# Optimization experiments

Hardware: AMD Instinct MI355X
Metric: run time of the kernel (lower is better)

The kernel has to match this reference:

```python
import jax, jax.numpy as jnp
import numpy as np

B, N_SNPS, N_GENES = 16, 500000, 20000
N_NODES, N_EDGES = 600000, 320000
NF, L = 8, 2
BN_EPS = 1e-5

def bn(x, g, b):
    # eval-mode BatchNorm1d with freshly-initialized running stats (mean=0, var=1)
    return x * jax.lax.rsqrt(jnp.float32(1.0) + BN_EPS) * g + b

def gelu(x):
    return jax.nn.gelu(x, approximate=False)  # torch F.gelu default (erf)

def setup_inputs():
    key = jax.random.key(0)
    ks = iter(jax.random.split(key, 40))
    nk = lambda: next(ks)
    lin = lambda kk, i, o: jax.random.normal(kk, (i, o), jnp.float32) * 0.02
    gam = lambda kk, n: 1.0 + 0.02 * jax.random.normal(kk, (n,), jnp.float32)
    inp = {}
    inp['snp'] = jax.random.uniform(nk(), (B, N_SNPS), jnp.float32)
    inp['snp_ids'] = jax.random.randint(nk(), (N_NODES,), 0, N_SNPS)
    inp['gene_of_node'] = jnp.sort(jax.random.randint(nk(), (N_NODES,), 0, N_GENES))
    inp['edge_src'] = jax.random.randint(nk(), (N_EDGES,), 0, N_GENES)
    inp['edge_dst'] = jax.random.randint(nk(), (N_EDGES,), 0, N_GENES)
    inp['filters'] = jax.random.normal(nk(), (NF, N_SNPS), jnp.float32) * 0.001
    inp['eps'] = jnp.zeros((L,), jnp.float32)  # GIN learn_eps, init 0
    inp['W1'] = jnp.stack([lin(nk(), NF, 2 * NF) for _ in range(L)])
    inp['b1'] = jnp.zeros((L, 2 * NF), jnp.float32)
    inp['g1'] = jnp.stack([gam(nk(), 2 * NF) for _ in range(L)])
    inp['bt1'] = jnp.zeros((L, 2 * NF), jnp.float32)
    inp['W2'] = jnp.stack([lin(nk(), 2 * NF, NF) for _ in range(L)])
    inp['b2'] = jnp.zeros((L, NF), jnp.float32)
    inp['g2'] = jnp.stack([gam(nk(), NF) for _ in range(L)])
    inp['bt2'] = jnp.zeros((L, NF), jnp.float32)
    inp['Wk'] = lin(nk(), NF, NF); inp['bk'] = jnp.zeros((NF,), jnp.float32)
    inp['Wq'] = lin(nk(), NF, 1)
    inp['Wv'] = lin(nk(), NF, NF); inp['bv'] = jnp.zeros((NF,), jnp.float32)
    inp['Wp1'] = lin(nk(), NF, 64); inp['bp1'] = jnp.zeros((64,), jnp.float32)
    inp['gp1'] = gam(nk(), 64); inp['btp1'] = jnp.zeros((64,), jnp.float32)
    inp['Wp2'] = lin(nk(), 64, 16); inp['bp2'] = jnp.zeros((16,), jnp.float32)
    inp['gp2'] = gam(nk(), 16); inp['btp2'] = jnp.zeros((16,), jnp.float32)
    inp['Wp3'] = lin(nk(), 16, 1); inp['bp3'] = jnp.zeros((1,), jnp.float32)
    return inp

def reference(snp, snp_ids, gene_of_node, edge_src, edge_dst, filters, eps,
              W1, b1, g1, bt1, W2, b2, g2, bt2,
              Wk, bk, Wq, Wv, bv,
              Wp1, bp1, gp1, btp1, Wp2, bp2, gp2, btp2, Wp3, bp3):
    # snp_h[b,n,f] = snp[b,n] * filters[f,n]  (concat of per-filter einsum 'bnd,n->bnd' with d=1)
    snp_h = snp[:, :, None] * filters.T[None]                      # [B, N_SNPS, NF]
    node_h = jnp.take(snp_h, snp_ids, axis=1)                      # [B, N_NODES, NF] gather per sample
    seg_gene = lambda x: jax.ops.segment_sum(x, gene_of_node, num_segments=N_GENES)
    h = jax.vmap(seg_gene)(node_h)                                 # [B, N_GENES, NF] SNP->gene readout
    seg_edge = lambda x: jax.ops.segment_sum(jnp.take(x, edge_src, axis=0), edge_dst, num_segments=N_GENES)
    for l in range(L):
        agg = jax.vmap(seg_edge)(h)                                # GIN sum aggregation on gene graph
        z = (1.0 + eps[l]) * h + agg
        z = gelu(bn(z @ W1[l] + b1[l], g1[l], bt1[l]))
        z = z @ W2[l] + b2[l]
        h = gelu(bn(z, g2[l], bt2[l]))
    # attentive readout: w = sigmoid(Wq(key(h))); graph feature = sum_nodes(value(h) * w)
    keys = h @ Wk + bk
    w = jax.nn.sigmoid(keys @ Wq)                                  # [B, N_GENES, 1]
    v = h @ Wv + bv
    g_h = jnp.sum(v * w, axis=1)                                   # [B, NF]
    z = gelu(bn(g_h @ Wp1 + bp1, gp1, btp1))
    z = gelu(bn(z @ Wp2 + bp2, gp2, btp2))
    preds = z @ Wp3 + bp3                                          # [B, 1]
    return preds, filters, w
```

## Files before the change

### kernel.cpp

```cpp
#include <hip/hip_runtime.h>
#include <math.h>

#define NSNPS  500000
#define NGENES 20000
#define NNODES 600000
#define NEDGES 320000
#define BB     16
#define NFILT  8
#define NBLK2  5000
#define MAXDEG 64

#define BN_SCALE 0.99999500003749968f

typedef unsigned short u16;

__device__ __forceinline__ float gelu_erf(float x) {
    return 0.5f * x * (1.0f + erff(x * 0.70710678118654752f));
}
__device__ __forceinline__ float sigmoidf_(float x) {
    return 1.0f / (1.0f + expf(-x));
}
__device__ __forceinline__ u16 f2bf(float x) {
    unsigned u = __float_as_uint(x);
    u += 0x7fffu + ((u >> 16) & 1u);
    return (u16)(u >> 16);
}
__device__ __forceinline__ float bf1(u16 v)      { return __uint_as_float(((unsigned)v) << 16); }
__device__ __forceinline__ float bflo(unsigned v){ return __uint_as_float(v << 16); }
__device__ __forceinline__ float bfhi(unsigned v){ return __uint_as_float(v & 0xffff0000u); }
__device__ __forceinline__ unsigned pack2(float a, float b) {
    return (unsigned)f2bf(a) | ((unsigned)f2bf(b) << 16);
}

#define KA_NA 1954
#define KA_NB 79
__global__ __launch_bounds__(256) void kA_prep(const float* __restrict__ snp,
                                               const float* __restrict__ filters,
                                               const int* __restrict__ gene_of_node,
                                               u16* __restrict__ nodeRow,
                                               float* __restrict__ out_filt,
                                               int* __restrict__ node_off,
                                               int* __restrict__ cursor,
                                               float* __restrict__ g_h4) {
    int bid = blockIdx.x;
    int t = threadIdx.x;

    if (bid < KA_NA) {
        int n = bid * 256 + t;
        if (n < NSNPS) {
            float f0 = filters[0 * NSNPS + n], f1 = filters[1 * NSNPS + n];
            float f2 = filters[2 * NSNPS + n], f3 = filters[3 * NSNPS + n];
            float f4 = filters[4 * NSNPS + n], f5 = filters[5 * NSNPS + n];
            float f6 = filters[6 * NSNPS + n], f7 = filters[7 * NSNPS + n];
            out_filt[0 * NSNPS + n] = f0; out_filt[1 * NSNPS + n] = f1;
            out_filt[2 * NSNPS + n] = f2; out_filt[3 * NSNPS + n] = f3;
            out_filt[4 * NSNPS + n] = f4; out_filt[5 * NSNPS + n] = f5;
            out_filt[6 * NSNPS + n] = f6; out_filt[7 * NSNPS + n] = f7;
            uint4 r0, r1, r2;
            r0.x = pack2(snp[0 * (size_t)NSNPS + n],  snp[1 * (size_t)NSNPS + n]);
            r0.y = pack2(snp[2 * (size_t)NSNPS + n],  snp[3 * (size_t)NSNPS + n]);
            r0.z = pack2(snp[4 * (size_t)NSNPS + n],  snp[5 * (size_t)NSNPS + n]);
            r0.w = pack2(snp[6 * (size_t)NSNPS + n],  snp[7 * (size_t)NSNPS + n]);
            r1.x = pack2(snp[8 * (size_t)NSNPS + n],  snp[9 * (size_t)NSNPS + n]);
            r1.y = pack2(snp[10 * (size_t)NSNPS + n], snp[11 * (size_t)NSNPS + n]);
            r1.z = pack2(snp[12 * (size_t)NSNPS + n], snp[13 * (size_t)NSNPS + n]);
            r1.w = pack2(snp[14 * (size_t)NSNPS + n], snp[15 * (size_t)NSNPS + n]);
            r2.x = pack2(f0, f1); r2.y = pack2(f2, f3);
            r2.z = pack2(f4, f5); r2.w = pack2(f6, f7);
            uint4* dst = (uint4*)(nodeRow + (size_t)n * 32);
            dst[0] = r0; dst[1] = r1; dst[2] = r2;
        }
        return;
    }
    int g = (bid - KA_NA) * 256 + t;
    if (g <= NGENES) {
        int lo = 0, hi = NNODES;
        while (lo < hi) {
            int mid = (lo + hi) >> 1;
            if (gene_of_node[mid] < g) lo = mid + 1; else hi = mid;
        }
        node_off[g] = lo;
    }
    if (g < NGENES) cursor[g] = g * MAXDEG;
    if (g < 512)    g_h4[g] = 0.0f;
}

#define KB_SCAT 1250
__global__ __launch_bounds__(256) void kB_gather(const u16* __restrict__ nodeRow,
                                                 const int* __restrict__ snp_ids,
                                                 const int* __restrict__ node_off,
                                                 const int* __restrict__ edge_src,
                                                 const int* __restrict__ edge_dst,
                                                 int* __restrict__ cursor,
                                                 int* __restrict__ csr_src,
                                                 u16* __restrict__ h_bf) {
    int bid = blockIdx.x;
    int t = threadIdx.x;
    if (bid >= NGENES) {
        int e = (bid - NGENES) * 256 + t;
        if (e < NEDGES) {
            int dst = edge_dst[e];
            int p = atomicAdd(&cursor[dst], 1);
            if (p < dst * MAXDEG + MAXDEG)
                csr_src[p] = edge_src[e];
        }
        return;
    }
    __shared__ float sZ[4][128];
    int g = bid;
    int wave = t >> 6, lane = t & 63;
    int sub = (wave << 2) + (lane >> 4);
    int b = lane & 15;
    int s = node_off[g], e = node_off[g + 1];

    float acc[8];
    #pragma unroll
    for (int f = 0; f < 8; f++) acc[f] = 0.0f;

    int i = s + sub;
    for (; i + 16 < e; i += 32) {
        int id0 = snp_ids[i];
        int id1 = snp_ids[i + 16];
        const u16* r0 = nodeRow + (size_t)id0 * 32;
        const u16* r1 = nodeRow + (size_t)id1 * 32;
        float v0 = bf1(r0[b]);
        float v1 = bf1(r1[b]);
        uint4 F0 = *(const uint4*)(r0 + 16);
        uint4 F1 = *(const uint4*)(r1 + 16);
        acc[0] += v0 * bflo(F0.x) + v1 * bflo(F1.x);
        acc[1] += v0 * bfhi(F0.x) + v1 * bfhi(F1.x);
        acc[2] += v0 * bflo(F0.y) + v1 * bflo(F1.y);
        acc[3] += v0 * bfhi(F0.y) + v1 * bfhi(F1.y);
        acc[4] += v0 * bflo(F0.z) + v1 * bflo(F1.z);
        acc[5] += v0 * bfhi(F0.z) + v1 * bfhi(F1.z);
        acc[6] += v0 * bflo(F0.w) + v1 * bflo(F1.w);
        acc[7] += v0 * bfhi(F0.w) + v1 * bfhi(F1.w);
    }
    if (i < e) {
        int id0 = snp_ids[i];
        const u16* r0 = nodeRow + (size_t)id0 * 32;
        float v0 = bf1(r0[b]);
        uint4 F0 = *(const uint4*)(r0 + 16);
        acc[0] += v0 * bflo(F0.x); acc[1] += v0 * bfhi(F0.x);
        acc[2] += v0 * bflo(F0.y); acc[3] += v0 * bfhi(F0.y);
        acc[4] += v0 * bflo(F0.z); acc[5] += v0 * bfhi(F0.z);
        acc[6] += v0 * bflo(F0.w); acc[7] += v0 * bfhi(F0.w);
    }
    #pragma unroll
    for (int f = 0; f < 8; f++) {
        acc[f] += __shfl_xor(acc[f], 16, 64);
        acc[f] += __shfl_xor(acc[f], 32, 64);
    }
    if (lane < 16) {
        float* dst = &sZ[wave][lane * 8];
        *(float4*)(dst)     = make_float4(acc[0], acc[1], acc[2], acc[3]);
        *(float4*)(dst + 4) = make_float4(acc[4], acc[5], acc[6], acc[7]);
    }
    __syncthreads();
    if (t < 128) {
        float val = sZ[0][t] + sZ[1][t] + sZ[2][t] + sZ[3][t];
        h_bf[(size_t)g * 128 + t] = f2bf(val);
    }
}

__global__ __launch_bounds__(256) void kC_gin1(const u16* __restrict__ hin,
                                               u16* __restrict__ hout,
                                               const int* __restrict__ cursor,
                                               const int* __restrict__ csr_src,
                                               const float* __restrict__ eps_l,
                                               const float* __restrict__ W1,
                                               const float* __restrict__ b1,
                                               const float* __restrict__ g1,
                                               const float* __restrict__ bt1,
                                               const float* __restrict__ W2,
                                               const float* __restrict__ b2,
                                               const float* __restrict__ g2,
                                               const float* __restrict__ bt2) {
    __shared__ float sW1[128], sb1[16], sg1[16], sbt1[16];
    __shared__ float sW2[128], sb2[8], sg2[8], sbt2[8];
    int t = threadIdx.x;
    if (t < 128) { sW1[t] = W1[t]; sW2[t] = W2[t]; }
    if (t < 16)  { sb1[t] = b1[t]; sg1[t] = g1[t]; sbt1[t] = bt1[t]; }
    if (t < 8)   { sb2[t] = b2[t]; sg2[t] = g2[t]; sbt2[t] = bt2[t]; }

    int chunk = blockIdx.x & 3;
    int g = (blockIdx.x >> 2) * 16 + (t >> 4);
    int u = t & 15;
    int half = u >> 3;
    int colpos = u & 7;
    int fh = colpos & 1;
    int jgroup = half * 2 + fh;
    int col = chunk * 32 + colpos * 4;
    const u16* __restrict__ hc = hin + col;
    float epsv = 1.0f + eps_l[0];

    float a0, a1, a2, a3;
    if (half == 0) {
        uint2 su = *(const uint2*)(hc + (size_t)g * 128);
        a0 = bflo(su.x) * epsv; a1 = bfhi(su.x) * epsv;
        a2 = bflo(su.y) * epsv; a3 = bfhi(su.y) * epsv;
    } else {
        a0 = a1 = a2 = a3 = 0.0f;
    }

    int s = g * MAXDEG;
    int e = cursor[g];
    e = (e < s + MAXDEG) ? e : (s + MAXDEG);
    int k = s + half;
    for (; k + 14 < e; k += 16) {
        int i0 = csr_src[k],      i1 = csr_src[k + 2];
        int i2 = csr_src[k + 4],  i3 = csr_src[k + 6];
        int i4 = csr_src[k + 8],  i5 = csr_src[k + 10];
        int i6 = csr_src[k + 12], i7 = csr_src[k + 14];
        uint2 v0 = *(const uint2*)(hc + (size_t)i0 * 128);
        uint2 v1 = *(const uint2*)(hc + (size_t)i1 * 128);
        uint2 v2 = *(const uint2*)(hc + (size_t)i2 * 128);
        uint2 v3 = *(const uint2*)(hc + (size_t)i3 * 128);
        uint2 v4 = *(const uint2*)(hc + (size_t)i4 * 128);
        uint2 v5 = *(const uint2*)(hc + (size_t)i5 * 128);
        uint2 v6 = *(const uint2*)(hc + (size_t)i6 * 128);
        uint2 v7 = *(const uint2*)(hc + (size_t)i7 * 128);
        a0 += ((bflo(v0.x) + bflo(v1.x)) + (bflo(v2.x) + bflo(v3.x)))
            + ((bflo(v4.x) + bflo(v5.x)) + (bflo(v6.x) + bflo(v7.x)));
        a1 += ((bfhi(v0.x) + bfhi(v1.x)) + (bfhi(v2.x) + bfhi(v3.x)))
            + ((bfhi(v4.x) + bfhi(v5.x)) + (bfhi(v6.x) + bfhi(v7.x)));
        a2 += ((bflo(v0.y) + bflo(v1.y)) + (bflo(v2.y) + bflo(v3.y)))
            + ((bflo(v4.y) + bflo(v5.y)) + (bflo(v6.y) + bflo(v7.y)));
        a3 += ((bfhi(v0.y) + bfhi(v1.y)) + (bfhi(v2.y) + bfhi(v3.y)))
            + ((bfhi(v4.y) + bfhi(v5.y)) + (bfhi(v6.y) + bfhi(v7.y)));
    }
    for (; k < e; k += 2) {
        int i0 = csr_src[k];
        uint2 v0 = *(const uint2*)(hc + (size_t)i0 * 128);
        a0 += bflo(v0.x); a1 += bfhi(v0.x);
        a2 += bflo(v0.y); a3 += bfhi(v0.y);
    }
    __syncthreads();

    a0 += __shfl_xor(a0, 8, 64);
    a1 += __shfl_xor(a1, 8, 64);
    a2 += __shfl_xor(a2, 8, 64);
    a3 += __shfl_xor(a3, 8, 64);
    float p0 = __shfl_xor(a0, 1, 64);
    float p1 = __shfl_xor(a1, 1, 64);
    float p2 = __shfl_xor(a2, 1, 64);
    float p3 = __shfl_xor(a3, 1, 64);
    float z[8];
    z[fh * 4 + 0] = a0; z[fh * 4 + 1] = a1; z[fh * 4 + 2] = a2; z[fh * 4 + 3] = a3;
    z[(1 - fh) * 4 + 0] = p0; z[(1 - fh) * 4 + 1] = p1;
    z[(1 - fh) * 4 + 2] = p2; z[(1 - fh) * 4 + 3] = p3;

    float op[8];
    #pragma unroll
    for (int f = 0; f < 8; f++) op[f] = (jgroup == 0) ? sb2[f] : 0.0f;
    #pragma unroll
    for (int jj = 0; jj < 4; jj++) {
        int j = jgroup * 4 + jj;
        float s1 = sb1[j];
        #pragma unroll
        for (int i2 = 0; i2 < 8; i2++) s1 += z[i2] * sW1[i2 * 16 + j];
        s1 = s1 * BN_SCALE * sg1[j] + sbt1[j];
        s1 = gelu_erf(s1);
        #pragma unroll
        for (int f = 0; f < 8; f++) op[f] += s1 * sW2[j * 8 + f];
    }
    float r[4];
    #pragma unroll
    for (int fi = 0; fi < 4; fi++) {
        int f = fh * 4 + fi;
        float x = op[f] + __shfl_xor(op[f], 1, 64);
        x += __shfl_xor(x, 8, 64);
        r[fi] = gelu_erf(x * BN_SCALE * sg2[f] + sbt2[f]);
    }
    if (half == 0) {
        uint2 ou;
        ou.x = pack2(r[0], r[1]); ou.y = pack2(r[2], r[3]);
        *(uint2*)(hout + (size_t)g * 128 + col) = ou;
    }
}

__global__ __launch_bounds__(256) void kD_gin2(const u16* __restrict__ hin,
                                               const int* __restrict__ cursor,
                                               const int* __restrict__ csr_src,
                                               const float* __restrict__ eps_l,
                                               const float* __restrict__ W1,
                                               const float* __restrict__ b1,
                                               const float* __restrict__ g1,
                                               const float* __restrict__ bt1,
                                               const float* __restrict__ W2,
                                               const float* __restrict__ b2,
                                               const float* __restrict__ g2,
                                               const float* __restrict__ bt2,
                                               const float* __restrict__ Wk,
                                               const float* __restrict__ bk,
                                               const float* __restrict__ Wq,
                                               const float* __restrict__ Wv,
                                               const float* __restrict__ bv,
                                               float* __restrict__ w_out,
                                               float* __restrict__ g_h4) {
    __shared__ float sW1[128], sb1[16], sg1[16], sbt1[16];
    __shared__ float sW2[128], sb2[8], sg2[8], sbt2[8];
    __shared__ float sWk[64], sWv[64], sbk[8], sbv[8], sWq[8];
    __shared__ float sRed[4][4][8];
    int t = threadIdx.x;
    if (t < 128) { sW1[t] = W1[t]; sW2[t] = W2[t]; }
    if (t < 64)  { sWk[t] = Wk[t]; sWv[t] = Wv[t]; }
    if (t < 16)  { sb1[t] = b1[t]; sg1[t] = g1[t]; sbt1[t] = bt1[t]; }
    if (t < 8)   { sb2[t] = b2[t]; sg2[t] = g2[t]; sbt2[t] = bt2[t];
                   sbk[t] = bk[t]; sbv[t] = bv[t]; sWq[t] = Wq[t]; }

    int chunk = blockIdx.x & 3;
    int g = (blockIdx.x >> 2) * 16 + (t >> 4);
    int u = t & 15;
    int half = u >> 3;
    int colpos = u & 7;
    int fh = colpos & 1;
    int jgroup = half * 2 + fh;
    int b = chunk * 4 + (colpos >> 1);
    int col = chunk * 32 + colpos * 4;
    const u16* __restrict__ hc = hin + col;
    float epsv = 1.0f + eps_l[0];

    float a0, a1, a2, a3;
    if (half == 0) {
        uint2 su = *(const uint2*)(hc + (size_t)g * 128);
        a0 = bflo(su.x) * epsv; a1 = bfhi(su.x) * epsv;
        a2 = bflo(su.y) * epsv; a3 = bfhi(su.y) * epsv;
    } else {
        a0 = a1 = a2 = a3 = 0.0f;
    }

    int s = g * MAXDEG;
    int e = cursor[g];
    e = (e < s + MAXDEG) ? e : (s + MAXDEG);
    int k = s + half;
    for (; k + 14 < e; k += 16) {
        int i0 = csr_src[k],      i1 = csr_src[k + 2];
        int i2 = csr_src[k + 4],  i3 = csr_src[k + 6];
        int i4 = csr_src[k + 8],  i5 = csr_src[k + 10];
        int i6 = csr_src[k + 12], i7 = csr_src[k + 14];
        uint2 v0 = *(const uint2*)(hc + (size_t)i0 * 128);
        uint2 v1 = *(const uint2*)(hc + (size_t)i1 * 128);
        uint2 v2 = *(const uint2*)(hc + (size_t)i2 * 128);
        uint2 v3 = *(const uint2*)(hc + (size_t)i3 * 128);
        uint2 v4 = *(const uint2*)(hc + (size_t)i4 * 128);
        uint2 v5 = *(const uint2*)(hc + (size_t)i5 * 128);
        uint2 v6 = *(const uint2*)(hc + (size_t)i6 * 128);
        uint2 v7 = *(const uint2*)(hc + (size_t)i7 * 128);
        a0 += ((bflo(v0.x) + bflo(v1.x)) + (bflo(v2.x) + bflo(v3.x)))
            + ((bflo(v4.x) + bflo(v5.x)) + (bflo(v6.x) + bflo(v7.x)));
        a1 += ((bfhi(v0.x) + bfhi(v1.x)) + (bfhi(v2.x) + bfhi(v3.x)))
            + ((bfhi(v4.x) + bfhi(v5.x)) + (bfhi(v6.x) + bfhi(v7.x)));
        a2 += ((bflo(v0.y) + bflo(v1.y)) + (bflo(v2.y) + bflo(v3.y)))
            + ((bflo(v4.y) + bflo(v5.y)) + (bflo(v6.y) + bflo(v7.y)));
        a3 += ((bfhi(v0.y) + bfhi(v1.y)) + (bfhi(v2.y) + bfhi(v3.y)))
            + ((bfhi(v4.y) + bfhi(v5.y)) + (bfhi(v6.y) + bfhi(v7.y)));
    }
    for (; k < e; k += 2) {
        int i0 = csr_src[k];
        uint2 v0 = *(const uint2*)(hc + (size_t)i0 * 128);
        a0 += bflo(v0.x); a1 += bfhi(v0.x);
        a2 += bflo(v0.y); a3 += bfhi(v0.y);
    }
    __syncthreads();

    a0 += __shfl_xor(a0, 8, 64);
    a1 += __shfl_xor(a1, 8, 64);
    a2 += __shfl_xor(a2, 8, 64);
    a3 += __shfl_xor(a3, 8, 64);
    float p0 = __shfl_xor(a0, 1, 64);
    float p1 = __shfl_xor(a1, 1, 64);
    float p2 = __shfl_xor(a2, 1, 64);
    float p3 = __shfl_xor(a3, 1, 64);
    float z[8];
    z[fh * 4 + 0] = a0; z[fh * 4 + 1] = a1; z[fh * 4 + 2] = a2; z[fh * 4 + 3] = a3;
    z[(1 - fh) * 4 + 0] = p0; z[(1 - fh) * 4 + 1] = p1;
    z[(1 - fh) * 4 + 2] = p2; z[(1 - fh) * 4 + 3] = p3;

    float op[8];
    #pragma unroll
    for (int f = 0; f < 8; f++) op[f] = (jgroup == 0) ? sb2[f] : 0.0f;
    #pragma unroll
    for (int jj = 0; jj < 4; jj++) {
        int j = jgroup * 4 + jj;
        float s1 = sb1[j];
        #pragma unroll
        for (int i2 = 0; i2 < 8; i2++) s1 += z[i2] * sW1[i2 * 16 + j];
        s1 = s1 * BN_SCALE * sg1[j] + sbt1[j];
        s1 = gelu_erf(s1);
        #pragma unroll
        for (int f = 0; f < 8; f++) op[f] += s1 * sW2[j * 8 + f];
    }
    float hvh[4];
    #pragma unroll
    for (int fi = 0; fi < 4; fi++) {
        int f = fh * 4 + fi;
        float x = op[f] + __shfl_xor(op[f], 1, 64);
        x += __shfl_xor(x, 8, 64);
        hvh[fi] = gelu_erf(x * BN_SCALE * sg2[f] + sbt2[f]);
    }
    float hv[8];
    #pragma unroll
    for (int fi = 0; fi < 4; fi++) {
        hv[fh * 4 + fi] = hvh[fi];
        hv[(1 - fh) * 4 + fi] = __shfl_xor(hvh[fi], 1, 64);
    }

    float qp = 0.0f;
    #pragma unroll
    for (int jj = 0; jj < 2; jj++) {
        int j = jgroup * 2 + jj;
        float key = sbk[j];
        #pragma unroll
        for (int i2 = 0; i2 < 8; i2++) key += hv[i2] * sWk[i2 * 8 + j];
        qp += key * sWq[j];
    }
    float q = qp + __shfl_xor(qp, 1, 64);
    q += __shfl_xor(q, 8, 64);
    float w = sigmoidf_(q);
    if (fh == 0 && half == 0) w_out[(size_t)b * NGENES + g] = w;

    float contrib[4];
    #pragma unroll
    for (int fi = 0; fi < 4; fi++) {
        int f = fh * 4 + fi;
        float v = sbv[f];
        #pragma unroll
        for (int i2 = 0; i2 < 8; i2++) v += hv[i2] * sWv[i2 * 8 + f];
        contrib[fi] = (half == 0) ? v * w : 0.0f;
    }
    #pragma unroll
    for (int fi = 0; fi < 4; fi++) {
        contrib[fi] += __shfl_xor(contrib[fi], 8, 64);
        contrib[fi] += __shfl_xor(contrib[fi], 16, 64);
        contrib[fi] += __shfl_xor(contrib[fi], 32, 64);
    }
    int wave = t >> 6, lane = t & 63;
    if (lane < 8) {
        #pragma unroll
        for (int fi = 0; fi < 4; fi++)
            sRed[wave][lane >> 1][(lane & 1) * 4 + fi] = contrib[fi];
    }
    __syncthreads();
    if (t < 32) {
        int bl = t >> 3, f = t & 7;
        float sm = sRed[0][bl][f] + sRed[1][bl][f] + sRed[2][bl][f] + sRed[3][bl][f];
        int shard = (blockIdx.x >> 2) & 3;
        atomicAdd(&g_h4[shard * 128 + (chunk * 4 + bl) * 8 + f], sm);
    }
}

__global__ __launch_bounds__(1024) void kE_head(const float* __restrict__ g_h4,
                                                const float* __restrict__ Wp1, const float* __restrict__ bp1,
                                                const float* __restrict__ gp1, const float* __restrict__ btp1,
                                                const float* __restrict__ Wp2, const float* __restrict__ bp2,
                                                const float* __restrict__ gp2, const float* __restrict__ btp2,
                                                const float* __restrict__ Wp3, const float* __restrict__ bp3,
                                                float* __restrict__ preds) {
    __shared__ float sgh[128];
    __shared__ float z1[16 * 64];
    __shared__ float z2[16 * 16];
    int t = threadIdx.x;
    if (t < 128) sgh[t] = (g_h4[t] + g_h4[128 + t]) + (g_h4[256 + t] + g_h4[384 + t]);
    __syncthreads();
    {
        int b = t >> 6, j = t & 63;
        float s = bp1[j];
        #pragma unroll
        for (int k = 0; k < 8; k++) s += sgh[b * 8 + k] * Wp1[k * 64 + j];
        s = s * BN_SCALE * gp1[j] + btp1[j];
        z1[b * 64 + j] = gelu_erf(s);
    }
    __syncthreads();
    if (t < 256) {
        int b = t >> 4, j = t & 15;
        float s = bp2[j];
        for (int k = 0; k < 64; k++) s += z1[b * 64 + k] * Wp2[k * 16 + j];
        s = s * BN_SCALE * gp2[j] + btp2[j];
        z2[b * 16 + j] = gelu_erf(s);
    }
    __syncthreads();
    if (t < 16) {
        float s = bp3[0];
        #pragma unroll
        for (int k = 0; k < 16; k++) s += z2[t * 16 + k] * Wp3[k];
        preds[t] = s;
    }
}

extern "C" void kernel_launch(void* const* d_in, const int* in_sizes, int n_in,
                              void* d_out, int out_size, void* d_ws, size_t ws_size,
                              hipStream_t stream) {
    const float* snp          = (const float*)d_in[0];
    const int*   snp_ids      = (const int*)  d_in[1];
    const int*   gene_of_node = (const int*)  d_in[2];
    const int*   edge_src     = (const int*)  d_in[3];
    const int*   edge_dst     = (const int*)  d_in[4];
    const float* filters      = (const float*)d_in[5];
    const float* eps          = (const float*)d_in[6];
    const float* W1  = (const float*)d_in[7];
    const float* b1  = (const float*)d_in[8];
    const float* g1  = (const float*)d_in[9];
    const float* bt1 = (const float*)d_in[10];
    const float* W2  = (const float*)d_in[11];
    const float* b2  = (const float*)d_in[12];
    const float* g2  = (const float*)d_in[13];
    const float* bt2 = (const float*)d_in[14];
    const float* Wk  = (const float*)d_in[15];
    const float* bk  = (const float*)d_in[16];
    const float* Wq  = (const float*)d_in[17];
    const float* Wv  = (const float*)d_in[18];
    const float* bv  = (const float*)d_in[19];
    const float* Wp1 = (const float*)d_in[20];
    const float* bp1 = (const float*)d_in[21];
    const float* gp1 = (const float*)d_in[22];
    const float* btp1= (const float*)d_in[23];
    const float* Wp2 = (const float*)d_in[24];
    const float* bp2 = (const float*)d_in[25];
    const float* gp2 = (const float*)d_in[26];
    const float* btp2= (const float*)d_in[27];
    const float* Wp3 = (const float*)d_in[28];
    const float* bp3 = (const float*)d_in[29];

    float* out        = (float*)d_out;
    float* out_preds  = out;
    float* out_filt   = out + 16;
    float* out_w      = out + 16 + NFILT * NSNPS;

    char* ws = (char*)d_ws;
    size_t off = 0;
    u16* nodeRow = (u16*)(ws + off); off += (size_t)NSNPS * 64;
    u16* h0   = (u16*)(ws + off); off += (size_t)NGENES * 128 * 2;
    u16* h1   = (u16*)(ws + off); off += (size_t)NGENES * 128 * 2;
    int* node_off = (int*)(ws + off); off += ((NGENES + 1) * 4 + 255) / 256 * 256;
    int* cursor   = (int*)(ws + off); off += (NGENES * 4 + 255) / 256 * 256;
    int* csr_src  = (int*)(ws + off); off += (size_t)NGENES * MAXDEG * 4;
    float* g_h4   = (float*)(ws + off); off += 4 * 128 * 4;

    kA_prep<<<KA_NA + KA_NB, 256, 0, stream>>>(
        snp, filters, gene_of_node, nodeRow, out_filt, node_off, cursor, g_h4);
    kB_gather<<<NGENES + KB_SCAT, 256, 0, stream>>>(
        nodeRow, snp_ids, node_off, edge_src, edge_dst, cursor, csr_src, h0);
    kC_gin1<<<NBLK2, 256, 0, stream>>>(h0, h1, cursor, csr_src, eps + 0,
                                       W1 + 0 * 128, b1 + 0 * 16, g1 + 0 * 16, bt1 + 0 * 16,
                                       W2 + 0 * 128, b2 + 0 * 8, g2 + 0 * 8, bt2 + 0 * 8);
    kD_gin2<<<NBLK2, 256, 0, stream>>>(h1, cursor, csr_src, eps + 1,
                                       W1 + 1 * 128, b1 + 1 * 16, g1 + 1 * 16, bt1 + 1 * 16,
                                       W2 + 1 * 128, b2 + 1 * 8, g2 + 1 * 8, bt2 + 1 * 8,
                                       Wk, bk, Wq, Wv, bv, out_w, g_h4);
    kE_head<<<1, 1024, 0, stream>>>(g_h4, Wp1, bp1, gp1, btp1,
                                    Wp2, bp2, gp2, btp2, Wp3, bp3, out_preds);
}
```

Before: 271.1 us.

## Map one wave per gene in SNP gather and widen atomic shards

The SNP-to-gene gather now assigns one 64-lane wave per gene instead of a 256-thread block per gene. Each wave unrolls four node rows per iteration, removing the shared-memory reduction and block barrier, and writes the bf16 gene row straight from registers. The edge-scatter blocks now come first in the grid, and the graph-level atomic accumulator is split into eight shards instead of four to reduce atomic contention. The trade-off is fewer lanes per gene, so load per wave grows for genes with many nodes, and the head kernel must sum more partial buffers.

```diff
diff --git a/kernel.cpp b/kernel.cpp
--- a/kernel.cpp
+++ b/kernel.cpp
@@ -41,7 +41,7 @@
                                                float* __restrict__ out_filt,
                                                int* __restrict__ node_off,
                                                int* __restrict__ cursor,
-                                               float* __restrict__ g_h4) {
+                                               float* __restrict__ g_h8) {
     int bid = blockIdx.x;
     int t = threadIdx.x;
 
@@ -82,10 +82,11 @@
         node_off[g] = lo;
     }
     if (g < NGENES) cursor[g] = g * MAXDEG;
-    if (g < 512)    g_h4[g] = 0.0f;
+    if (g < 1024)   g_h8[g] = 0.0f;
 }
 
 #define KB_SCAT 1250
+#define KB_GATH 5000
 __global__ __launch_bounds__(256) void kB_gather(const u16* __restrict__ nodeRow,
                                                  const int* __restrict__ snp_ids,
                                                  const int* __restrict__ node_off,
@@ -96,8 +97,8 @@
                                                  u16* __restrict__ h_bf) {
     int bid = blockIdx.x;
     int t = threadIdx.x;
-    if (bid >= NGENES) {
-        int e = (bid - NGENES) * 256 + t;
+    if (bid < KB_SCAT) {
+        int e = bid * 256 + t;
         if (e < NEDGES) {
             int dst = edge_dst[e];
             int p = atomicAdd(&cursor[dst], 1);
@@ -106,10 +107,9 @@
         }
         return;
     }
-    __shared__ float sZ[4][128];
-    int g = bid;
     int wave = t >> 6, lane = t & 63;
-    int sub = (wave << 2) + (lane >> 4);
+    int g = (bid - KB_SCAT) * 4 + wave;
+    int slot = lane >> 4;
     int b = lane & 15;
     int s = node_off[g], e = node_off[g + 1];
 
@@ -117,10 +117,36 @@
     #pragma unroll
     for (int f = 0; f < 8; f++) acc[f] = 0.0f;
 
-    int i = s + sub;
-    for (; i + 16 < e; i += 32) {
+    int i = s + slot;
+    for (; i + 12 < e; i += 16) {
         int id0 = snp_ids[i];
-        int id1 = snp_ids[i + 16];
+        int id1 = snp_ids[i + 4];
+        int id2 = snp_ids[i + 8];
+        int id3 = snp_ids[i + 12];
+        const u16* r0 = nodeRow + (size_t)id0 * 32;
+        const u16* r1 = nodeRow + (size_t)id1 * 32;
+        const u16* r2 = nodeRow + (size_t)id2 * 32;
+        const u16* r3 = nodeRow + (size_t)id3 * 32;
+        float v0 = bf1(r0[b]);
+        float v1 = bf1(r1[b]);
+        float v2 = bf1(r2[b]);
+        float v3 = bf1(r3[b]);
+        uint4 F0 = *(const uint4*)(r0 + 16);
+        uint4 F1 = *(const uint4*)(r1 + 16);
+        uint4 F2 = *(const uint4*)(r2 + 16);
+        uint4 F3 = *(const uint4*)(r3 + 16);
+        acc[0] += (v0 * bflo(F0.x) + v1 * bflo(F1.x)) + (v2 * bflo(F2.x) + v3 * bflo(F3.x));
+        acc[1] += (v0 * bfhi(F0.x) + v1 * bfhi(F1.x)) + (v2 * bfhi(F2.x) + v3 * bfhi(F3.x));
+        acc[2] += (v0 * bflo(F0.y) + v1 * bflo(F1.y)) + (v2 * bflo(F2.y) + v3 * bflo(F3.y));
+        acc[3] += (v0 * bfhi(F0.y) + v1 * bfhi(F1.y)) + (v2 * bfhi(F2.y) + v3 * bfhi(F3.y));
+        acc[4] += (v0 * bflo(F0.z) + v1 * bflo(F1.z)) + (v2 * bflo(F2.z) + v3 * bflo(F3.z));
+        acc[5] += (v0 * bfhi(F0.z) + v1 * bfhi(F1.z)) + (v2 * bfhi(F2.z) + v3 * bfhi(F3.z));
+        acc[6] += (v0 * bflo(F0.w) + v1 * bflo(F1.w)) + (v2 * bflo(F2.w) + v3 * bflo(F3.w));
+        acc[7] += (v0 * bfhi(F0.w) + v1 * bfhi(F1.w)) + (v2 * bfhi(F2.w) + v3 * bfhi(F3.w));
+    }
+    for (; i + 4 < e; i += 8) {
+        int id0 = snp_ids[i];
+        int id1 = snp_ids[i + 4];
         const u16* r0 = nodeRow + (size_t)id0 * 32;
         const u16* r1 = nodeRow + (size_t)id1 * 32;
         float v0 = bf1(r0[b]);
@@ -152,14 +178,10 @@
         acc[f] += __shfl_xor(acc[f], 32, 64);
     }
     if (lane < 16) {
-        float* dst = &sZ[wave][lane * 8];
-        *(float4*)(dst)     = make_float4(acc[0], acc[1], acc[2], acc[3]);
-        *(float4*)(dst + 4) = make_float4(acc[4], acc[5], acc[6], acc[7]);
-    }
-    __syncthreads();
-    if (t < 128) {
-        float val = sZ[0][t] + sZ[1][t] + sZ[2][t] + sZ[3][t];
-        h_bf[(size_t)g * 128 + t] = f2bf(val);
+        uint4 o;
+        o.x = pack2(acc[0], acc[1]); o.y = pack2(acc[2], acc[3]);
+        o.z = pack2(acc[4], acc[5]); o.w = pack2(acc[6], acc[7]);
+        *(uint4*)(h_bf + (size_t)g * 128 + lane * 8) = o;
     }
 }
 
@@ -297,7 +319,7 @@
                                                const float* __restrict__ Wv,
                                                const float* __restrict__ bv,
                                                float* __restrict__ w_out,
-                                               float* __restrict__ g_h4) {
+                                               float* __restrict__ g_h8) {
     __shared__ float sW1[128], sb1[16], sg1[16], sbt1[16];
     __shared__ float sW2[128], sb2[8], sg2[8], sbt2[8];
     __shared__ float sWk[64], sWv[64], sbk[8], sbv[8], sWq[8];
@@ -445,12 +467,12 @@
     if (t < 32) {
         int bl = t >> 3, f = t & 7;
         float sm = sRed[0][bl][f] + sRed[1][bl][f] + sRed[2][bl][f] + sRed[3][bl][f];
-        int shard = (blockIdx.x >> 2) & 3;
-        atomicAdd(&g_h4[shard * 128 + (chunk * 4 + bl) * 8 + f], sm);
-    }
-}
-
-__global__ __launch_bounds__(1024) void kE_head(const float* __restrict__ g_h4,
+        int shard = (blockIdx.x >> 2) & 7;
+        atomicAdd(&g_h8[shard * 128 + (chunk * 4 + bl) * 8 + f], sm);
+    }
+}
+
+__global__ __launch_bounds__(1024) void kE_head(const float* __restrict__ g_h8,
                                                 const float* __restrict__ Wp1, const float* __restrict__ bp1,
                                                 const float* __restrict__ gp1, const float* __restrict__ btp1,
                                                 const float* __restrict__ Wp2, const float* __restrict__ bp2,
@@ -461,7 +483,13 @@
     __shared__ float z1[16 * 64];
     __shared__ float z2[16 * 16];
     int t = threadIdx.x;
-    if (t < 128) sgh[t] = (g_h4[t] + g_h4[128 + t]) + (g_h4[256 + t] + g_h4[384 + t]);
+    if (t < 128) {
+        float s01 = g_h8[t]           + g_h8[128 + t];
+        float s23 = g_h8[256 + t]     + g_h8[384 + t];
+        float s45 = g_h8[512 + t]     + g_h8[640 + t];
+        float s67 = g_h8[768 + t]     + g_h8[896 + t];
+        sgh[t] = (s01 + s23) + (s45 + s67);
+    }
     __syncthreads();
     {
         int b = t >> 6, j = t & 63;
@@ -535,11 +563,11 @@
     int* node_off = (int*)(ws + off); off += ((NGENES + 1) * 4 + 255) / 256 * 256;
     int* cursor   = (int*)(ws + off); off += (NGENES * 4 + 255) / 256 * 256;
     int* csr_src  = (int*)(ws + off); off += (size_t)NGENES * MAXDEG * 4;
-    float* g_h4   = (float*)(ws + off); off += 4 * 128 * 4;
+    float* g_h8   = (float*)(ws + off); off += 8 * 128 * 4;
 
     kA_prep<<<KA_NA + KA_NB, 256, 0, stream>>>(
-        snp, filters, gene_of_node, nodeRow, out_filt, node_off, cursor, g_h4);
-    kB_gather<<<NGENES + KB_SCAT, 256, 0, stream>>>(
+        snp, filters, gene_of_node, nodeRow, out_filt, node_off, cursor, g_h8);
+    kB_gather<<<KB_SCAT + KB_GATH, 256, 0, stream>>>(
         nodeRow, snp_ids, node_off, edge_src, edge_dst, cursor, csr_src, h0);
     kC_gin1<<<NBLK2, 256, 0, stream>>>(h0, h1, cursor, csr_src, eps + 0,
                                        W1 + 0 * 128, b1 + 0 * 16, g1 + 0 * 16, bt1 + 0 * 16,
@@ -547,7 +575,7 @@
     kD_gin2<<<NBLK2, 256, 0, stream>>>(h1, cursor, csr_src, eps + 1,
                                        W1 + 1 * 128, b1 + 1 * 16, g1 + 1 * 16, bt1 + 1 * 16,
                                        W2 + 1 * 128, b2 + 1 * 8, g2 + 1 * 8, bt2 + 1 * 8,
-                                       Wk, bk, Wq, Wv, bv, out_w, g_h4);
-    kE_head<<<1, 1024, 0, stream>>>(g_h4, Wp1, bp1, gp1, btp1,
+                                       Wk, bk, Wq, Wv, bv, out_w, g_h8);
+    kE_head<<<1, 1024, 0, stream>>>(g_h8, Wp1, bp1, gp1, btp1,
                                     Wp2, bp2, gp2, btp2, Wp3, bp3, out_preds);
 }
```

Result: faster. 261.4 us (median of 2 runs) (-3.6%).
